# Optimization experiments

Hardware: AMD Instinct MI355X
Metric: run time of the kernel (lower is better)

The kernel has to match this reference:

```python
import jax, jax.numpy as jnp
import numpy as np

A = 5            # num_anchors
NC = 20          # num_classes
IGNORE_THRESH = 0.6
COORD_SCALE = 1.0
NOOBJ_SCALE = 1.0
OBJ_SCALE = 5.0
CLASS_SCALE = 1.0
ANCHORS_NP = np.array([[0.052, 0.066], [0.14, 0.11], [0.24, 0.30], [0.45, 0.42], [0.77, 0.72]], dtype=np.float32)


def setup_inputs() -> dict:
    key = jax.random.key(0)
    k1, k2, k3, k4, k5 = jax.random.split(key, 5)
    B, F, O = 32, 38, 50
    C = A * (5 + NC)
    outputs = jax.random.normal(k1, (B, C, F, F), jnp.float32)
    # targets: (cx, cy, w, h, cls) normalized; padded rows are all-zero
    cxy = jax.random.uniform(k2, (B, O, 2), minval=0.15, maxval=0.85)
    wh = jax.random.uniform(k3, (B, O, 2), minval=0.05, maxval=0.20)
    cls = jax.random.randint(k4, (B, O), 0, NC).astype(jnp.float32)
    targets = jnp.concatenate([cxy, wh, cls[..., None]], axis=-1)
    nobj = jax.random.randint(k5, (B,), 10, O + 1)
    valid = (jnp.arange(O)[None, :] < nobj[:, None]).astype(jnp.float32)
    targets = targets * valid[..., None]
    return {"outputs": outputs, "targets": targets, "anchors": jnp.asarray(ANCHORS_NP)}


def _pairwise_iou_xywh(a, b):
    # a: (..., N, 4), b: (..., M, 4) center-format -> IoU (..., N, M)
    a = a[..., :, None, :]
    b = b[..., None, :, :]
    tl = jnp.maximum(a[..., :2] - a[..., 2:] * 0.5, b[..., :2] - b[..., 2:] * 0.5)
    br = jnp.minimum(a[..., :2] + a[..., 2:] * 0.5, b[..., :2] + b[..., 2:] * 0.5)
    wh = jnp.clip(br - tl, 0.0)
    inter = wh[..., 0] * wh[..., 1]
    area_a = a[..., 2] * a[..., 3]
    area_b = b[..., 2] * b[..., 3]
    return inter / (area_a + area_b - inter + 1e-12)


def _forward(outputs, targets, anchors):
    B, C, F, _ = outputs.shape
    S = F * F
    O = targets.shape[1]
    valid = targets.sum(axis=2) > 0                    # (B, O)
    gt = targets[..., :4] * F                          # grid-unit cxywh
    gt_cls = targets[..., 4]

    out5 = outputs.reshape(B, A, 5 + NC, F, F)
    jj = jnp.arange(F, dtype=outputs.dtype)            # x (last axis)
    ii = jnp.arange(F, dtype=outputs.dtype)[:, None]   # y
    aw = (anchors[:, 0] * F)[None, :, None, None]
    ah = (anchors[:, 1] * F)[None, :, None, None]
    px = jax.nn.sigmoid(out5[:, :, 0]) + jj
    py = jax.nn.sigmoid(out5[:, :, 1]) + ii
    pw = jnp.exp(out5[:, :, 2]) * aw
    ph = jnp.exp(out5[:, :, 3]) * ah
    pred_boxes = jnp.stack([px, py, pw, ph], -1).transpose(0, 2, 3, 1, 4).reshape(B, S * A, 4)

    # anchor prior boxes at cell centers: (S, A, 4)
    ax = jnp.broadcast_to(jj + 0.5, (F, F))
    ay = jnp.broadcast_to(ii + 0.5, (F, F))
    aa = jnp.stack([
        jnp.broadcast_to(ax[:, :, None], (F, F, A)),
        jnp.broadcast_to(ay[:, :, None], (F, F, A)),
        jnp.broadcast_to((anchors[:, 0] * F)[None, None, :], (F, F, A)),
        jnp.broadcast_to((anchors[:, 1] * F)[None, None, :], (F, F, A)),
    ], -1).reshape(S, A, 4)

    ious = _pairwise_iou_xywh(pred_boxes, gt)          # (B, S*A, O)
    ious = jnp.where(valid[:, None, :], ious, 0.0)     # padded objs excluded (IoU >= 0)
    max_iou = ious.reshape(B, S, A, O).max(axis=-1)    # (B, S, A)

    n_pos = jnp.any(max_iou > IGNORE_THRESH, axis=(1, 2))
    iou_mask = jnp.full((B, S, A), NOOBJ_SCALE, outputs.dtype)
    iou_mask = jnp.where(n_pos[:, None, None] & (max_iou >= IGNORE_THRESH), 0.0, iou_mask)

    overlaps = _pairwise_iou_xywh(aa.reshape(1, S * A, 4), gt).reshape(B, S, A, O)

    # responsible cell: floor of top-left corner (faithful to source), anchor = argmax prior overlap
    x1y1 = gt[..., :2] - gt[..., 2:] * 0.5
    cxcy = jnp.floor(x1y1).astype(jnp.int32)
    cell = jnp.clip(cxcy[..., 1] * F + cxcy[..., 0], 0, S - 1)             # (B, O)
    ovT = overlaps.transpose(0, 3, 1, 2)                                   # (B, O, S, A)
    ov_cell = jnp.take_along_axis(ovT, cell[:, :, None, None], axis=2)[:, :, 0, :]
    anchor_idx = jnp.argmax(ov_cell, axis=-1)                              # (B, O)
    resp = aa[cell, anchor_idx]                                            # (B, O, 4)
    deltas = jnp.stack([gt[..., 0] - resp[..., 0], gt[..., 1] - resp[..., 1],
                        gt[..., 2] / resp[..., 2], gt[..., 3] / resp[..., 3]], -1)
    mi = jnp.take_along_axis(jnp.take_along_axis(max_iou, cell[:, :, None], axis=1),
                             anchor_idx[:, :, None], axis=2)[..., 0]       # (B, O)

    b_rep = jnp.broadcast_to(jnp.arange(B)[:, None], (B, O))
    cell_s = jnp.where(valid, cell, S)  # OOB index for padded objs -> dropped
    zt = jnp.zeros((B, S, A), outputs.dtype)
    box_target = jnp.zeros((B, S, A, 4), outputs.dtype).at[b_rep, cell_s, anchor_idx].set(deltas, mode='drop')
    box_mask = zt.at[b_rep, cell_s, anchor_idx].set(1.0, mode='drop')
    class_target = zt.at[b_rep, cell_s, anchor_idx].set(gt_cls, mode='drop')
    class_mask = zt.at[b_rep, cell_s, anchor_idx].set(1.0, mode='drop')
    iou_target = zt.at[b_rep, cell_s, anchor_idx].set(mi, mode='drop')
    iou_mask = iou_mask.at[b_rep, cell_s, anchor_idx].set(OBJ_SCALE, mode='drop')

    # prediction side, layout (B, (i*F+j)*A + a, 5+NC) matching target layout
    outs = out5.transpose(0, 3, 4, 1, 2).reshape(B, S * A, 5 + NC)
    pd = jnp.concatenate([jax.nn.sigmoid(outs[..., :2]), jnp.exp(outs[..., 2:4])], -1)
    conf = jax.nn.sigmoid(outs[..., 4])
    probs = jax.nn.softmax(outs[..., 5:], axis=-1)

    bm = box_mask.reshape(B, S * A, 1)
    im = iou_mask.reshape(B, S * A)
    box_loss = jnp.sum((pd * bm - box_target.reshape(B, S * A, 4) * bm) ** 2)
    iou_loss = jnp.sum((conf * im - iou_target.reshape(B, S * A) * im) ** 2)
    # faithful quirk of the source: cross-entropy applied to softmax *outputs* as logits
    ls = jax.nn.log_softmax(probs, axis=-1)
    ct = class_target.reshape(B, S * A).astype(jnp.int32)
    ce = -jnp.take_along_axis(ls, ct[..., None], axis=-1)[..., 0]
    class_loss = jnp.sum(ce * class_mask.reshape(B, S * A))
    return (COORD_SCALE * box_loss + iou_loss + CLASS_SCALE * class_loss) / B


def reference(outputs, targets, anchors):
    return _forward(outputs, targets, anchors)
```

## Files before the change

kernel.cpp:

```cpp
#include <hip/hip_runtime.h>
#include <math.h>

#define A_N 5
#define NC 20
#define FD 38
#define SD (FD*FD)
#define BD 32
#define OD 50
#define SA (SD*A_N)
#define GX ((SA + 255) / 256)
#define IGN_T 0.6f
#define OBJ_S 5.0f

__device__ __forceinline__ float sigm(float x) { return 1.0f / (1.0f + expf(-x)); }

__global__ __launch_bounds__(256) void k_main(
    const float* __restrict__ outputs, const float* __restrict__ targets,
    const float* __restrict__ anchors,
    float* __restrict__ pbase, float* __restrict__ pcorr, int* __restrict__ pflag)
{
    __shared__ float g_tlx[OD], g_tly[OD], g_brx[OD], g_bry[OD], g_den[OD];
    __shared__ int   s_cnt, s_any;
    __shared__ int   s_key[OD], s_cls[OD];
    __shared__ float s_gx[OD], s_gy[OD], s_gw[OD], s_gh[OD];
    __shared__ float wb[4], wc[4];

    const int b = blockIdx.y;
    const int tid = threadIdx.x;
    if (tid == 0) { s_cnt = 0; s_any = 0; }
    __syncthreads();

    if (tid < OD) {
        const float* t = targets + (b * OD + tid) * 5;
        float tx = t[0], ty = t[1], tw = t[2], th = t[3], tc = t[4];
        int key = -1;
        if (tx + ty + tw + th + tc > 0.0f) {
            float gx = tx * FD, gy = ty * FD, gw = tw * FD, gh = th * FD;
            float gtlx = gx - gw * 0.5f, gtly = gy - gh * 0.5f;
            float gbrx = gx + gw * 0.5f, gbry = gy + gh * 0.5f;
            int k = atomicAdd(&s_cnt, 1);
            g_tlx[k] = gtlx; g_tly[k] = gtly;
            g_brx[k] = gbrx; g_bry[k] = gbry;
            g_den[k] = gw * gh + 1e-12f;
            int cx = (int)floorf(gtlx), cy = (int)floorf(gtly);
            int cell = min(max(cy * FD + cx, 0), SD - 1);
            int ci = cell / FD, cj = cell - ci * FD;
            float acx = (float)cj + 0.5f, acy = (float)ci + 0.5f;
            float areaB = gw * gh;
            float best = -1.0f; int bi = 0;
            for (int a = 0; a < A_N; ++a) {
                float aw = anchors[2 * a] * FD, ah = anchors[2 * a + 1] * FD;
                float w = fmaxf(fminf(acx + aw * 0.5f, gbrx) - fmaxf(acx - aw * 0.5f, gtlx), 0.0f);
                float h = fmaxf(fminf(acy + ah * 0.5f, gbry) - fmaxf(acy - ah * 0.5f, gtly), 0.0f);
                float inter = w * h;
                float iou = inter / (aw * ah + areaB - inter + 1e-12f);
                if (iou > best) { best = iou; bi = a; }
            }
            key = bi * SD + cell;
            s_gx[tid] = gx; s_gy[tid] = gy; s_gw[tid] = gw; s_gh[tid] = gh;
            s_cls[tid] = (int)tc;
        }
        s_key[tid] = key;
    }
    __syncthreads();
    const int cnt = s_cnt;

    const int idx = blockIdx.x * 256 + tid;
    float base = 0.0f, corr = 0.0f;
    bool hot = false;
    if (idx < SA) {
        const int a = idx / SD;
        const int s = idx - a * SD;
        const int i = s / FD, j = s - i * FD;
        const float* ob = outputs + ((size_t)b * (A_N * (5 + NC)) + a * (5 + NC)) * SD + s;
        float o0 = ob[0 * SD], o1 = ob[1 * SD], o2 = ob[2 * SD], o3 = ob[3 * SD];
        float cr = ob[4 * SD];
        float aw = anchors[2 * a] * FD, ah = anchors[2 * a + 1] * FD;
        float px = sigm(o0) + (float)j;
        float py = sigm(o1) + (float)i;
        float pw = expf(o2) * aw;
        float ph = expf(o3) * ah;
        float ptlx = px - pw * 0.5f, ptly = py - ph * 0.5f;
        float pbrx = px + pw * 0.5f, pbry = py + ph * 0.5f;
        float areaA = pw * ph;

        float m = 0.0f;
        for (int o = 0; o < cnt; ++o) {
            float w = fmaxf(fminf(pbrx, g_brx[o]) - fmaxf(ptlx, g_tlx[o]), 0.0f);
            float h = fmaxf(fminf(pbry, g_bry[o]) - fmaxf(ptly, g_tly[o]), 0.0f);
            float inter = w * h;
            float iou = inter / (areaA + g_den[o] - inter);
            m = fmaxf(m, iou);
        }
        hot = (m > IGN_T);

        int ro = -1;
        #pragma unroll 10
        for (int o = 0; o < OD; ++o) ro = (s_key[o] == idx) ? o : ro;

        float conf = sigm(cr);
        if (ro >= 0) {
            float d = conf - m;
            base += OBJ_S * OBJ_S * d * d;
            float dx = s_gx[ro] - ((float)j + 0.5f);
            float dy = s_gy[ro] - ((float)i + 0.5f);
            float dw = s_gw[ro] / aw;
            float dh = s_gh[ro] / ah;
            float e0 = sigm(o0) - dx;
            float e1 = sigm(o1) - dy;
            float e2 = expf(o2) - dw;
            float e3 = expf(o3) - dh;
            base += e0*e0 + e1*e1 + e2*e2 + e3*e3;
            int ct = s_cls[ro];
            float x[NC];
            float xmax = -INFINITY;
            #pragma unroll
            for (int k = 0; k < NC; ++k) { x[k] = ob[(5 + k) * SD]; xmax = fmaxf(xmax, x[k]); }
            float esum = 0.0f;
            #pragma unroll
            for (int k = 0; k < NC; ++k) { x[k] = expf(x[k] - xmax); esum += x[k]; }
            float inv = 1.0f / esum;
            float pmax = 0.0f, pct = 0.0f;
            #pragma unroll
            for (int k = 0; k < NC; ++k) {
                float p = x[k] * inv; x[k] = p;
                pmax = fmaxf(pmax, p);
                pct = (k == ct) ? p : pct;
            }
            float e2s = 0.0f;
            #pragma unroll
            for (int k = 0; k < NC; ++k) e2s += expf(x[k] - pmax);
            base += -(pct - (pmax + logf(e2s)));
        } else {
            float c2 = conf * conf;
            if (m < IGN_T) base += c2;
            else           corr += c2;
        }
    }

    unsigned long long bal = __ballot(hot);
    if ((tid & 63) == 0 && bal) atomicOr(&s_any, 1);

    #pragma unroll
    for (int off = 32; off > 0; off >>= 1) {
        base += __shfl_down(base, off);
        corr += __shfl_down(corr, off);
    }
    int lane = tid & 63, w = tid >> 6;
    if (lane == 0) { wb[w] = base; wc[w] = corr; }
    __syncthreads();
    if (tid == 0) {
        int gid = b * GX + blockIdx.x;
        pbase[gid] = wb[0] + wb[1] + wb[2] + wb[3];
        pcorr[gid] = wc[0] + wc[1] + wc[2] + wc[3];
        pflag[gid] = s_any;
    }
}

__global__ __launch_bounds__(256) void k_finish(
    const float* __restrict__ pbase, const float* __restrict__ pcorr,
    const int* __restrict__ pflag, float* __restrict__ out)
{
    __shared__ int npos[BD];
    __shared__ float wsum[4];
    const int tid = threadIdx.x;
    if (tid < BD) {
        int f = 0;
        for (int x = 0; x < GX; ++x) f |= pflag[tid * GX + x];
        npos[tid] = f;
    }
    __syncthreads();
    float sum = 0.0f;
    for (int g = tid; g < BD * GX; g += 256) {
        int b = g / GX;
        sum += pbase[g] + (npos[b] ? 0.0f : pcorr[g]);
    }
    #pragma unroll
    for (int off = 32; off > 0; off >>= 1) sum += __shfl_down(sum, off);
    int lane = tid & 63, w = tid >> 6;
    if (lane == 0) wsum[w] = sum;
    __syncthreads();
    if (tid == 0) out[0] = (wsum[0] + wsum[1] + wsum[2] + wsum[3]) * (1.0f / (float)BD);
}

extern "C" void kernel_launch(void* const* d_in, const int* in_sizes, int n_in,
                              void* d_out, int out_size, void* d_ws, size_t ws_size,
                              hipStream_t stream) {
    (void)in_sizes; (void)n_in; (void)out_size; (void)ws_size;
    const float* outputs = (const float*)d_in[0];
    const float* targets = (const float*)d_in[1];
    const float* anchors = (const float*)d_in[2];
    float* out = (float*)d_out;

    const int G = BD * GX;
    float* pbase = (float*)d_ws;
    float* pcorr = pbase + G;
    int*   pflag = (int*)(pcorr + G);

    k_main<<<dim3(GX, BD), 256, 0, stream>>>(outputs, targets, anchors,
                                             pbase, pcorr, pflag);
    k_finish<<<dim3(1), 256, 0, stream>>>(pbase, pcorr, pflag, out);
}
```

Before: 85.98 us.

## Process two anchor cells per thread and stage targets in shared memory

Each thread now handles two prediction positions (idx and idx+HALF), so every shared-memory ground-truth box loaded in the IoU loop is reused for two predictions and the grid is halved. The output loads are issued before the first barrier, which overlaps global latency with target setup, and targets and anchors are staged through shared memory. The max-IoU tracking now uses cross-multiplied comparisons to avoid a division per ground truth, and sigmoid, exp and log switch to fast intrinsics. The trade-offs are lower precision from the intrinsics, higher register pressure, and fewer blocks available for latency hiding.

```diff
diff --git a/kernel.cpp b/kernel.cpp
--- a/kernel.cpp
+++ b/kernel.cpp
@@ -8,39 +8,105 @@
 #define BD 32
 #define OD 50
 #define SA (SD*A_N)
-#define GX ((SA + 255) / 256)
+#define HALF (SA/2)
+#define GX ((HALF + 255) / 256)
+#define NBLK (BD * GX)
 #define IGN_T 0.6f
 #define OBJ_S 5.0f
 
-__device__ __forceinline__ float sigm(float x) { return 1.0f / (1.0f + expf(-x)); }
+__device__ __forceinline__ float sigm(float x) { return 1.0f / (1.0f + __expf(-x)); }
+
+__device__ __forceinline__ void accum_loss(
+    const float* __restrict__ ob, float m, int ro,
+    float sx, float sy, float ew, float eh, float conf,
+    float jj, float ii, float aw, float ah,
+    const float* s_gx, const float* s_gy, const float* s_gw, const float* s_gh,
+    const int* s_cls, float& base, float& corr)
+{
+    if (ro >= 0) {
+        float d = conf - m;
+        base += OBJ_S * OBJ_S * d * d;
+        float dx = s_gx[ro] - (jj + 0.5f);
+        float dy = s_gy[ro] - (ii + 0.5f);
+        float dw = s_gw[ro] / aw;
+        float dh = s_gh[ro] / ah;
+        float e0 = sx - dx, e1 = sy - dy, e2 = ew - dw, e3 = eh - dh;
+        base += e0*e0 + e1*e1 + e2*e2 + e3*e3;
+        int ct = s_cls[ro];
+        float x[NC];
+        float xmax = -INFINITY;
+        #pragma unroll
+        for (int k = 0; k < NC; ++k) { x[k] = ob[(5 + k) * SD]; xmax = fmaxf(xmax, x[k]); }
+        float esum = 0.0f;
+        #pragma unroll
+        for (int k = 0; k < NC; ++k) { x[k] = __expf(x[k] - xmax); esum += x[k]; }
+        float inv = 1.0f / esum;
+        float pmax = 0.0f, pct = 0.0f;
+        #pragma unroll
+        for (int k = 0; k < NC; ++k) {
+            float p = x[k] * inv; x[k] = p;
+            pmax = fmaxf(pmax, p);
+            pct = (k == ct) ? p : pct;
+        }
+        float e2s = 0.0f;
+        #pragma unroll
+        for (int k = 0; k < NC; ++k) e2s += __expf(x[k] - pmax);
+        base += -(pct - (pmax + __logf(e2s)));
+    } else {
+        float c2 = conf * conf;
+        if (m < IGN_T) base += c2;
+        else           corr += c2;
+    }
+}
 
 __global__ __launch_bounds__(256) void k_main(
     const float* __restrict__ outputs, const float* __restrict__ targets,
     const float* __restrict__ anchors,
     float* __restrict__ pbase, float* __restrict__ pcorr, int* __restrict__ pflag)
 {
-    __shared__ float g_tlx[OD], g_tly[OD], g_brx[OD], g_bry[OD], g_den[OD];
-    __shared__ int   s_cnt, s_any;
-    __shared__ int   s_key[OD], s_cls[OD];
-    __shared__ float s_gx[OD], s_gy[OD], s_gw[OD], s_gh[OD];
-    __shared__ float wb[4], wc[4];
+    __shared__ float4 g_box[OD];
+    __shared__ float  g_den[OD];
+    __shared__ float  s_traw[OD * 5];
+    __shared__ float  s_anc[2 * A_N];
+    __shared__ int    s_cnt, s_any;
+    __shared__ int    s_key[OD], s_cls[OD];
+    __shared__ float  s_gx[OD], s_gy[OD], s_gw[OD], s_gh[OD];
+    __shared__ float  wb[4], wc[4];
 
     const int b = blockIdx.y;
     const int tid = threadIdx.x;
     if (tid == 0) { s_cnt = 0; s_any = 0; }
+    if (tid < OD * 5)  s_traw[tid] = targets[b * (OD * 5) + tid];
+    if (tid < 2 * A_N) s_anc[tid]  = anchors[tid];
+
+    const int ix = blockIdx.x * 256 + tid;
+    const bool act = (ix < HALF);
+    const int p0 = ix, p1 = ix + HALF;
+    int a0 = p0 / SD, r0 = p0 - a0 * SD;
+    int a1 = p1 / SD, r1 = p1 - a1 * SD;
+    int ii0 = r0 / FD, jj0 = r0 - ii0 * FD;
+    int ii1 = r1 / FD, jj1 = r1 - ii1 * FD;
+    const float* ob0 = outputs + ((size_t)b * (A_N * (5 + NC)) + a0 * (5 + NC)) * SD + r0;
+    const float* ob1 = outputs + ((size_t)b * (A_N * (5 + NC)) + a1 * (5 + NC)) * SD + r1;
+    float q00 = 0, q01 = 0, q02 = 0, q03 = 0, q04 = 0;
+    float q10 = 0, q11 = 0, q12 = 0, q13 = 0, q14 = 0;
+    if (act) {
+        q00 = ob0[0]; q01 = ob0[SD]; q02 = ob0[2 * SD]; q03 = ob0[3 * SD]; q04 = ob0[4 * SD];
+        q10 = ob1[0]; q11 = ob1[SD]; q12 = ob1[2 * SD]; q13 = ob1[3 * SD]; q14 = ob1[4 * SD];
+    }
     __syncthreads();
 
     if (tid < OD) {
-        const float* t = targets + (b * OD + tid) * 5;
-        float tx = t[0], ty = t[1], tw = t[2], th = t[3], tc = t[4];
+        float tx = s_traw[tid * 5 + 0], ty = s_traw[tid * 5 + 1];
+        float tw = s_traw[tid * 5 + 2], th = s_traw[tid * 5 + 3];
+        float tc = s_traw[tid * 5 + 4];
         int key = -1;
         if (tx + ty + tw + th + tc > 0.0f) {
             float gx = tx * FD, gy = ty * FD, gw = tw * FD, gh = th * FD;
             float gtlx = gx - gw * 0.5f, gtly = gy - gh * 0.5f;
             float gbrx = gx + gw * 0.5f, gbry = gy + gh * 0.5f;
             int k = atomicAdd(&s_cnt, 1);
-            g_tlx[k] = gtlx; g_tly[k] = gtly;
-            g_brx[k] = gbrx; g_bry[k] = gbry;
+            g_box[k] = make_float4(gtlx, gtly, gbrx, gbry);
             g_den[k] = gw * gh + 1e-12f;
             int cx = (int)floorf(gtlx), cy = (int)floorf(gtly);
             int cell = min(max(cy * FD + cx, 0), SD - 1);
@@ -49,7 +115,7 @@
             float areaB = gw * gh;
             float best = -1.0f; int bi = 0;
             for (int a = 0; a < A_N; ++a) {
-                float aw = anchors[2 * a] * FD, ah = anchors[2 * a + 1] * FD;
+                float aw = s_anc[2 * a] * FD, ah = s_anc[2 * a + 1] * FD;
                 float w = fmaxf(fminf(acx + aw * 0.5f, gbrx) - fmaxf(acx - aw * 0.5f, gtlx), 0.0f);
                 float h = fmaxf(fminf(acy + ah * 0.5f, gbry) - fmaxf(acy - ah * 0.5f, gtly), 0.0f);
                 float inter = w * h;
@@ -65,77 +131,53 @@
     __syncthreads();
     const int cnt = s_cnt;
 
-    const int idx = blockIdx.x * 256 + tid;
     float base = 0.0f, corr = 0.0f;
     bool hot = false;
-    if (idx < SA) {
-        const int a = idx / SD;
-        const int s = idx - a * SD;
-        const int i = s / FD, j = s - i * FD;
-        const float* ob = outputs + ((size_t)b * (A_N * (5 + NC)) + a * (5 + NC)) * SD + s;
-        float o0 = ob[0 * SD], o1 = ob[1 * SD], o2 = ob[2 * SD], o3 = ob[3 * SD];
-        float cr = ob[4 * SD];
-        float aw = anchors[2 * a] * FD, ah = anchors[2 * a + 1] * FD;
-        float px = sigm(o0) + (float)j;
-        float py = sigm(o1) + (float)i;
-        float pw = expf(o2) * aw;
-        float ph = expf(o3) * ah;
-        float ptlx = px - pw * 0.5f, ptly = py - ph * 0.5f;
-        float pbrx = px + pw * 0.5f, pbry = py + ph * 0.5f;
-        float areaA = pw * ph;
-
-        float m = 0.0f;
+    if (act) {
+        float aw0 = s_anc[2 * a0] * FD, ah0 = s_anc[2 * a0 + 1] * FD;
+        float aw1 = s_anc[2 * a1] * FD, ah1 = s_anc[2 * a1 + 1] * FD;
+        float sx0 = sigm(q00), sy0 = sigm(q01), ew0 = __expf(q02), eh0 = __expf(q03);
+        float sx1 = sigm(q10), sy1 = sigm(q11), ew1 = __expf(q12), eh1 = __expf(q13);
+        float pw0 = ew0 * aw0, ph0 = eh0 * ah0;
+        float pw1 = ew1 * aw1, ph1 = eh1 * ah1;
+        float px0 = sx0 + (float)jj0, py0 = sy0 + (float)ii0;
+        float px1 = sx1 + (float)jj1, py1 = sy1 + (float)ii1;
+        float tlx0 = px0 - pw0 * 0.5f, tly0 = py0 - ph0 * 0.5f;
+        float brx0 = px0 + pw0 * 0.5f, bry0 = py0 + ph0 * 0.5f;
+        float tlx1 = px1 - pw1 * 0.5f, tly1 = py1 - ph1 * 0.5f;
+        float brx1 = px1 + pw1 * 0.5f, bry1 = py1 + ph1 * 0.5f;
+        float ar0 = pw0 * ph0, ar1 = pw1 * ph1;
+
+        float bn0 = 0.0f, bd0 = 1.0f, bn1 = 0.0f, bd1 = 1.0f;
         for (int o = 0; o < cnt; ++o) {
-            float w = fmaxf(fminf(pbrx, g_brx[o]) - fmaxf(ptlx, g_tlx[o]), 0.0f);
-            float h = fmaxf(fminf(pbry, g_bry[o]) - fmaxf(ptly, g_tly[o]), 0.0f);
-            float inter = w * h;
-            float iou = inter / (areaA + g_den[o] - inter);
-            m = fmaxf(m, iou);
-        }
-        hot = (m > IGN_T);
-
-        int ro = -1;
+            float4 bx = g_box[o];
+            float  dn = g_den[o];
+            float w0 = fmaxf(fminf(brx0, bx.z) - fmaxf(tlx0, bx.x), 0.0f);
+            float h0 = fmaxf(fminf(bry0, bx.w) - fmaxf(tly0, bx.y), 0.0f);
+            float in0 = w0 * h0, de0 = ar0 + dn - in0;
+            if (in0 * bd0 > bn0 * de0) { bn0 = in0; bd0 = de0; }
+            float w1 = fmaxf(fminf(brx1, bx.z) - fmaxf(tlx1, bx.x), 0.0f);
+            float h1 = fmaxf(fminf(bry1, bx.w) - fmaxf(tly1, bx.y), 0.0f);
+            float in1 = w1 * h1, de1 = ar1 + dn - in1;
+            if (in1 * bd1 > bn1 * de1) { bn1 = in1; bd1 = de1; }
+        }
+        float m0 = bn0 / bd0, m1 = bn1 / bd1;
+        hot = (m0 > IGN_T) || (m1 > IGN_T);
+
+        int ro0 = -1, ro1 = -1;
         #pragma unroll 10
-        for (int o = 0; o < OD; ++o) ro = (s_key[o] == idx) ? o : ro;
-
-        float conf = sigm(cr);
-        if (ro >= 0) {
-            float d = conf - m;
-            base += OBJ_S * OBJ_S * d * d;
-            float dx = s_gx[ro] - ((float)j + 0.5f);
-            float dy = s_gy[ro] - ((float)i + 0.5f);
-            float dw = s_gw[ro] / aw;
-            float dh = s_gh[ro] / ah;
-            float e0 = sigm(o0) - dx;
-            float e1 = sigm(o1) - dy;
-            float e2 = expf(o2) - dw;
-            float e3 = expf(o3) - dh;
-            base += e0*e0 + e1*e1 + e2*e2 + e3*e3;
-            int ct = s_cls[ro];
-            float x[NC];
-            float xmax = -INFINITY;
-            #pragma unroll
-            for (int k = 0; k < NC; ++k) { x[k] = ob[(5 + k) * SD]; xmax = fmaxf(xmax, x[k]); }
-            float esum = 0.0f;
-            #pragma unroll
-            for (int k = 0; k < NC; ++k) { x[k] = expf(x[k] - xmax); esum += x[k]; }
-            float inv = 1.0f / esum;
-            float pmax = 0.0f, pct = 0.0f;
-            #pragma unroll
-            for (int k = 0; k < NC; ++k) {
-                float p = x[k] * inv; x[k] = p;
-                pmax = fmaxf(pmax, p);
-                pct = (k == ct) ? p : pct;
-            }
-            float e2s = 0.0f;
-            #pragma unroll
-            for (int k = 0; k < NC; ++k) e2s += expf(x[k] - pmax);
-            base += -(pct - (pmax + logf(e2s)));
-        } else {
-            float c2 = conf * conf;
-            if (m < IGN_T) base += c2;
-            else           corr += c2;
-        }
+        for (int o = 0; o < OD; ++o) {
+            int k = s_key[o];
+            ro0 = (k == p0) ? o : ro0;
+            ro1 = (k == p1) ? o : ro1;
+        }
+        float conf0 = sigm(q04), conf1 = sigm(q14);
+        accum_loss(ob0, m0, ro0, sx0, sy0, ew0, eh0, conf0,
+                   (float)jj0, (float)ii0, aw0, ah0,
+                   s_gx, s_gy, s_gw, s_gh, s_cls, base, corr);
+        accum_loss(ob1, m1, ro1, sx1, sy1, ew1, eh1, conf1,
+                   (float)jj1, (float)ii1, aw1, ah1,
+                   s_gx, s_gy, s_gw, s_gh, s_cls, base, corr);
     }
 
     unsigned long long bal = __ballot(hot);
@@ -171,9 +213,9 @@
     }
     __syncthreads();
     float sum = 0.0f;
-    for (int g = tid; g < BD * GX; g += 256) {
-        int b = g / GX;
-        sum += pbase[g] + (npos[b] ? 0.0f : pcorr[g]);
+    for (int g = tid; g < NBLK; g += 256) {
+        int bb = g / GX;
+        sum += pbase[g] + (npos[bb] ? 0.0f : pcorr[g]);
     }
     #pragma unroll
     for (int off = 32; off > 0; off >>= 1) sum += __shfl_down(sum, off);
@@ -192,10 +234,9 @@
     const float* anchors = (const float*)d_in[2];
     float* out = (float*)d_out;
 
-    const int G = BD * GX;
     float* pbase = (float*)d_ws;
-    float* pcorr = pbase + G;
-    int*   pflag = (int*)(pcorr + G);
+    float* pcorr = pbase + NBLK;
+    int*   pflag = (int*)(pcorr + NBLK);
 
     k_main<<<dim3(GX, BD), 256, 0, stream>>>(outputs, targets, anchors,
                                              pbase, pcorr, pflag);
```

New measurement: 82.50 us. 1.04x faster.
